# Kernel tuning notes

Hardware: AMD Instinct MI355X
Metric: run time of the kernel (lower is better)

## Reference

```python
import jax, jax.numpy as jnp
import numpy as np

WORDS_CNT = 34835
EMBED_DIM = 512
NEG = -1e30  # stand-in for -inf that is safe under autodiff


def setup_inputs() -> dict:
    key = jax.random.key(0)
    k1, k2, k3, k4, k5 = jax.random.split(key, 5)
    B, Tt, Td = 2048, 30, 150
    title = jax.random.randint(k1, (B, Tt), 0, WORDS_CNT + 1, dtype=jnp.int64)
    desc = jax.random.randint(k2, (B, Td), 0, WORDS_CNT + 1, dtype=jnp.int64)
    t_len = jax.random.randint(k3, (B,), 0, Tt + 1, dtype=jnp.int64)
    d_len = jax.random.randint(k4, (B,), 0, Td + 1, dtype=jnp.int64)
    word2vec = jax.random.normal(k5, (WORDS_CNT + 1, EMBED_DIM), dtype=jnp.float32)
    word2vec = word2vec.at[0].set(0.0)  # padding_idx=0
    return {"title": title, "desc": desc, "t_len": t_len, "d_len": d_len,
            "mode": 0, "word2vec": word2vec}


def _pool(vec, lens):
    # vec: [B, T, D], lens: [B] -> (max_pool [B, D], mean_pool [B, D])
    T = vec.shape[1]
    mask = (jnp.arange(T)[None, :] < lens[:, None])  # [B, T]
    m3 = mask[:, :, None]
    mx = jnp.max(jnp.where(m3, vec, NEG), axis=1)
    nonempty = (lens > 0)[:, None]
    mx = jnp.where(nonempty, mx, 0.0)
    denom = jnp.maximum(lens, 1).astype(vec.dtype)[:, None]
    mean = jnp.sum(jnp.where(m3, vec, 0.0), axis=1) / denom
    mean = jnp.where(nonempty, mean, 0.0)
    return mx, mean


def reference(title, desc, t_len, d_len, mode, word2vec):
    title_vec = word2vec[title]  # [B, Tt, D]
    desc_vec = word2vec[desc]    # [B, Td, D]
    t_max, t_avg = _pool(title_vec, t_len)
    d_max, d_avg = _pool(desc_vec, d_len)
    return jnp.concatenate([t_max, d_max, t_avg, d_avg], axis=1)  # [B, 4*D]
```

## Files before the change

kernel.cpp:

```cpp
#include <hip/hip_runtime.h>

#define TT 30
#define TD 150
#define NEGV -1e30f

__global__ __launch_bounds__(128) void swem_pool_kernel(
    const int* __restrict__ title, const int* __restrict__ desc,
    const int* __restrict__ t_len, const int* __restrict__ d_len,
    const float4* __restrict__ w2v, float4* __restrict__ out)
{
    __shared__ int s_idx[TT + TD];
    const int b = blockIdx.x;
    const int tid = threadIdx.x;

    if (tid < TT) s_idx[tid] = title[b * TT + tid];
    for (int i = tid; i < TD; i += 128) s_idx[TT + i] = desc[b * TD + i];
    __syncthreads();

    const int tl = t_len[b];
    const int dl = d_len[b];

    float4 mx = make_float4(NEGV, NEGV, NEGV, NEGV);
    float4 sm = make_float4(0.f, 0.f, 0.f, 0.f);
    for (int t = 0; t < tl; ++t) {
        const float4 v = w2v[(size_t)s_idx[t] * 128 + tid];
        mx.x = fmaxf(mx.x, v.x); mx.y = fmaxf(mx.y, v.y);
        mx.z = fmaxf(mx.z, v.z); mx.w = fmaxf(mx.w, v.w);
        sm.x += v.x; sm.y += v.y; sm.z += v.z; sm.w += v.w;
    }
    float4 tmax, tavg;
    if (tl > 0) {
        const float inv = 1.0f / (float)tl;
        tmax = mx;
        tavg = make_float4(sm.x * inv, sm.y * inv, sm.z * inv, sm.w * inv);
    } else {
        tmax = make_float4(0.f, 0.f, 0.f, 0.f);
        tavg = make_float4(0.f, 0.f, 0.f, 0.f);
    }

    mx = make_float4(NEGV, NEGV, NEGV, NEGV);
    sm = make_float4(0.f, 0.f, 0.f, 0.f);
    for (int t = 0; t < dl; ++t) {
        const float4 v = w2v[(size_t)s_idx[TT + t] * 128 + tid];
        mx.x = fmaxf(mx.x, v.x); mx.y = fmaxf(mx.y, v.y);
        mx.z = fmaxf(mx.z, v.z); mx.w = fmaxf(mx.w, v.w);
        sm.x += v.x; sm.y += v.y; sm.z += v.z; sm.w += v.w;
    }
    float4 dmax, davg;
    if (dl > 0) {
        const float inv = 1.0f / (float)dl;
        dmax = mx;
        davg = make_float4(sm.x * inv, sm.y * inv, sm.z * inv, sm.w * inv);
    } else {
        dmax = make_float4(0.f, 0.f, 0.f, 0.f);
        davg = make_float4(0.f, 0.f, 0.f, 0.f);
    }

    float4* orow = out + (size_t)b * 512;
    orow[tid]       = tmax;
    orow[128 + tid] = dmax;
    orow[256 + tid] = tavg;
    orow[384 + tid] = davg;
}

extern "C" void kernel_launch(void* const* d_in, const int* in_sizes, int n_in,
                              void* d_out, int out_size, void* d_ws, size_t ws_size,
                              hipStream_t stream) {
    const int* title = (const int*)d_in[0];
    const int* desc  = (const int*)d_in[1];
    const int* t_len = (const int*)d_in[2];
    const int* d_len = (const int*)d_in[3];
    const float4* w2v = (const float4*)d_in[5];

    float4* out = (float4*)d_out;

    const int B = in_sizes[2];
    swem_pool_kernel<<<B, 128, 0, stream>>>(title, desc, t_len, d_len, w2v, out);
}
```

Measured before the change: 148.9 us.

## Split title/desc into separate blocks and parallelize token loop across four groups

Launches a 2D grid so title and description pooling run in separate blocks. Each block uses 512 threads split into four groups that stride over tokens, then combines their partial max and sum through shared memory. The aim is more memory-level parallelism and fewer serial dependent gathers per thread, which should hide latency better. The cost is an extra shared-memory reduction and barrier, plus some idle groups on short title sequences.

```diff
diff --git a/kernel.cpp b/kernel.cpp
--- a/kernel.cpp
+++ b/kernel.cpp
@@ -3,64 +3,70 @@
 #define TT 30
 #define TD 150
 #define NEGV -1e30f
+#define NGRP 4
+#define LANES 128
 
-__global__ __launch_bounds__(128) void swem_pool_kernel(
+__global__ __launch_bounds__(512) void swem_pool_kernel(
     const int* __restrict__ title, const int* __restrict__ desc,
     const int* __restrict__ t_len, const int* __restrict__ d_len,
     const float4* __restrict__ w2v, float4* __restrict__ out)
 {
-    __shared__ int s_idx[TT + TD];
-    const int b = blockIdx.x;
-    const int tid = threadIdx.x;
+    __shared__ int s_idx[TD];
+    __shared__ float red[8][NGRP][LANES];
 
-    if (tid < TT) s_idx[tid] = title[b * TT + tid];
-    for (int i = tid; i < TD; i += 128) s_idx[TT + i] = desc[b * TD + i];
+    const int b    = blockIdx.x;
+    const int seg  = blockIdx.y;
+    const int tid  = threadIdx.x;
+    const int lane = tid & (LANES - 1);
+    const int grp  = tid >> 7;
+
+    const int* toks   = seg ? (desc + b * TD) : (title + b * TT);
+    const int  maxlen = seg ? TD : TT;
+    const int  len    = seg ? d_len[b] : t_len[b];
+
+    for (int i = tid; i < maxlen; i += 512) s_idx[i] = toks[i];
     __syncthreads();
-
-    const int tl = t_len[b];
-    const int dl = d_len[b];
 
     float4 mx = make_float4(NEGV, NEGV, NEGV, NEGV);
     float4 sm = make_float4(0.f, 0.f, 0.f, 0.f);
-    for (int t = 0; t < tl; ++t) {
-        const float4 v = w2v[(size_t)s_idx[t] * 128 + tid];
+    #pragma unroll 4
+    for (int t = grp; t < len; t += NGRP) {
+        const float4 v = w2v[(size_t)s_idx[t] * 128 + lane];
         mx.x = fmaxf(mx.x, v.x); mx.y = fmaxf(mx.y, v.y);
         mx.z = fmaxf(mx.z, v.z); mx.w = fmaxf(mx.w, v.w);
         sm.x += v.x; sm.y += v.y; sm.z += v.z; sm.w += v.w;
     }
-    float4 tmax, tavg;
-    if (tl > 0) {
-        const float inv = 1.0f / (float)tl;
-        tmax = mx;
-        tavg = make_float4(sm.x * inv, sm.y * inv, sm.z * inv, sm.w * inv);
-    } else {
-        tmax = make_float4(0.f, 0.f, 0.f, 0.f);
-        tavg = make_float4(0.f, 0.f, 0.f, 0.f);
-    }
 
-    mx = make_float4(NEGV, NEGV, NEGV, NEGV);
-    sm = make_float4(0.f, 0.f, 0.f, 0.f);
-    for (int t = 0; t < dl; ++t) {
-        const float4 v = w2v[(size_t)s_idx[TT + t] * 128 + tid];
-        mx.x = fmaxf(mx.x, v.x); mx.y = fmaxf(mx.y, v.y);
-        mx.z = fmaxf(mx.z, v.z); mx.w = fmaxf(mx.w, v.w);
-        sm.x += v.x; sm.y += v.y; sm.z += v.z; sm.w += v.w;
-    }
-    float4 dmax, davg;
-    if (dl > 0) {
-        const float inv = 1.0f / (float)dl;
-        dmax = mx;
-        davg = make_float4(sm.x * inv, sm.y * inv, sm.z * inv, sm.w * inv);
-    } else {
-        dmax = make_float4(0.f, 0.f, 0.f, 0.f);
-        davg = make_float4(0.f, 0.f, 0.f, 0.f);
-    }
+    red[0][grp][lane] = mx.x; red[1][grp][lane] = mx.y;
+    red[2][grp][lane] = mx.z; red[3][grp][lane] = mx.w;
+    red[4][grp][lane] = sm.x; red[5][grp][lane] = sm.y;
+    red[6][grp][lane] = sm.z; red[7][grp][lane] = sm.w;
+    __syncthreads();
 
     float4* orow = out + (size_t)b * 512;
-    orow[tid]       = tmax;
-    orow[128 + tid] = dmax;
-    orow[256 + tid] = tavg;
-    orow[384 + tid] = davg;
+
+    if (grp == 0) {
+        float4 r;
+        r.x = fmaxf(fmaxf(red[0][0][lane], red[0][1][lane]),
+                    fmaxf(red[0][2][lane], red[0][3][lane]));
+        r.y = fmaxf(fmaxf(red[1][0][lane], red[1][1][lane]),
+                    fmaxf(red[1][2][lane], red[1][3][lane]));
+        r.z = fmaxf(fmaxf(red[2][0][lane], red[2][1][lane]),
+                    fmaxf(red[2][2][lane], red[2][3][lane]));
+        r.w = fmaxf(fmaxf(red[3][0][lane], red[3][1][lane]),
+                    fmaxf(red[3][2][lane], red[3][3][lane]));
+        if (len == 0) r = make_float4(0.f, 0.f, 0.f, 0.f);
+        orow[seg * 128 + lane] = r;
+    } else if (grp == 1) {
+        const float inv = 1.0f / (float)(len > 0 ? len : 1);
+        float4 r;
+        r.x = (red[4][0][lane] + red[4][1][lane] + red[4][2][lane] + red[4][3][lane]) * inv;
+        r.y = (red[5][0][lane] + red[5][1][lane] + red[5][2][lane] + red[5][3][lane]) * inv;
+        r.z = (red[6][0][lane] + red[6][1][lane] + red[6][2][lane] + red[6][3][lane]) * inv;
+        r.w = (red[7][0][lane] + red[7][1][lane] + red[7][2][lane] + red[7][3][lane]) * inv;
+        if (len == 0) r = make_float4(0.f, 0.f, 0.f, 0.f);
+        orow[256 + seg * 128 + lane] = r;
+    }
 }
 
 extern "C" void kernel_launch(void* const* d_in, const int* in_sizes, int n_in,
@@ -73,7 +79,8 @@
     const float4* w2v = (const float4*)d_in[5];
 
     float4* out = (float4*)d_out;
+    const int B = in_sizes[2];
 
-    const int B = in_sizes[2];
-    swem_pool_kernel<<<B, 128, 0, stream>>>(title, desc, t_len, d_len, w2v, out);
+    dim3 grid(B, 2);
+    swem_pool_kernel<<<grid, 512, 0, stream>>>(title, desc, t_len, d_len, w2v, out);
 }
```

Result: no change. 148.6 us (-0.2%).

## Split title and desc pooling into separate blocks and unroll gather loop by 8

Applied to the files above, without the earlier changes.

Launches a 2D grid so that one block pools the title tokens and another pools the description tokens for each batch row, doubling the number of blocks. It also unrolls the token gather loop by eight so each thread has several independent row loads in flight. Both changes aim to hide gather latency, which is the main cost in this memory-bound embedding lookup. The trade-off is more blocks, load imbalance between the short title blocks and the long description blocks, and extra register pressure from the unrolled loads.

```diff
diff --git a/kernel.cpp b/kernel.cpp
--- a/kernel.cpp
+++ b/kernel.cpp
@@ -9,58 +9,58 @@
     const int* __restrict__ t_len, const int* __restrict__ d_len,
     const float4* __restrict__ w2v, float4* __restrict__ out)
 {
-    __shared__ int s_idx[TT + TD];
-    const int b = blockIdx.x;
+    __shared__ int s_idx[TD];
+
+    const int b   = blockIdx.x;
+    const int seg = blockIdx.y;
     const int tid = threadIdx.x;
 
-    if (tid < TT) s_idx[tid] = title[b * TT + tid];
-    for (int i = tid; i < TD; i += 128) s_idx[TT + i] = desc[b * TD + i];
+    const int* toks   = seg ? (desc + b * TD) : (title + b * TT);
+    const int  maxlen = seg ? TD : TT;
+    const int  len    = seg ? d_len[b] : t_len[b];
+
+    for (int i = tid; i < maxlen; i += 128) s_idx[i] = toks[i];
     __syncthreads();
-
-    const int tl = t_len[b];
-    const int dl = d_len[b];
 
     float4 mx = make_float4(NEGV, NEGV, NEGV, NEGV);
     float4 sm = make_float4(0.f, 0.f, 0.f, 0.f);
-    for (int t = 0; t < tl; ++t) {
+
+#define ACC(v) \
+    mx.x = fmaxf(mx.x, v.x); mx.y = fmaxf(mx.y, v.y); \
+    mx.z = fmaxf(mx.z, v.z); mx.w = fmaxf(mx.w, v.w); \
+    sm.x += v.x; sm.y += v.y; sm.z += v.z; sm.w += v.w;
+
+    int t = 0;
+    for (; t + 8 <= len; t += 8) {
+        const float4 v0 = w2v[(size_t)s_idx[t + 0] * 128 + tid];
+        const float4 v1 = w2v[(size_t)s_idx[t + 1] * 128 + tid];
+        const float4 v2 = w2v[(size_t)s_idx[t + 2] * 128 + tid];
+        const float4 v3 = w2v[(size_t)s_idx[t + 3] * 128 + tid];
+        const float4 v4 = w2v[(size_t)s_idx[t + 4] * 128 + tid];
+        const float4 v5 = w2v[(size_t)s_idx[t + 5] * 128 + tid];
+        const float4 v6 = w2v[(size_t)s_idx[t + 6] * 128 + tid];
+        const float4 v7 = w2v[(size_t)s_idx[t + 7] * 128 + tid];
+        ACC(v0) ACC(v1) ACC(v2) ACC(v3) ACC(v4) ACC(v5) ACC(v6) ACC(v7)
+    }
+    for (; t < len; ++t) {
         const float4 v = w2v[(size_t)s_idx[t] * 128 + tid];
-        mx.x = fmaxf(mx.x, v.x); mx.y = fmaxf(mx.y, v.y);
-        mx.z = fmaxf(mx.z, v.z); mx.w = fmaxf(mx.w, v.w);
-        sm.x += v.x; sm.y += v.y; sm.z += v.z; sm.w += v.w;
+        ACC(v)
     }
-    float4 tmax, tavg;
-    if (tl > 0) {
-        const float inv = 1.0f / (float)tl;
-        tmax = mx;
-        tavg = make_float4(sm.x * inv, sm.y * inv, sm.z * inv, sm.w * inv);
+#undef ACC
+
+    float4 rmax, ravg;
+    if (len > 0) {
+        const float inv = 1.0f / (float)len;
+        rmax = mx;
+        ravg = make_float4(sm.x * inv, sm.y * inv, sm.z * inv, sm.w * inv);
     } else {
-        tmax = make_float4(0.f, 0.f, 0.f, 0.f);
-        tavg = make_float4(0.f, 0.f, 0.f, 0.f);
-    }
-
-    mx = make_float4(NEGV, NEGV, NEGV, NEGV);
-    sm = make_float4(0.f, 0.f, 0.f, 0.f);
-    for (int t = 0; t < dl; ++t) {
-        const float4 v = w2v[(size_t)s_idx[TT + t] * 128 + tid];
-        mx.x = fmaxf(mx.x, v.x); mx.y = fmaxf(mx.y, v.y);
-        mx.z = fmaxf(mx.z, v.z); mx.w = fmaxf(mx.w, v.w);
-        sm.x += v.x; sm.y += v.y; sm.z += v.z; sm.w += v.w;
-    }
-    float4 dmax, davg;
-    if (dl > 0) {
-        const float inv = 1.0f / (float)dl;
-        dmax = mx;
-        davg = make_float4(sm.x * inv, sm.y * inv, sm.z * inv, sm.w * inv);
-    } else {
-        dmax = make_float4(0.f, 0.f, 0.f, 0.f);
-        davg = make_float4(0.f, 0.f, 0.f, 0.f);
+        rmax = make_float4(0.f, 0.f, 0.f, 0.f);
+        ravg = make_float4(0.f, 0.f, 0.f, 0.f);
     }
 
     float4* orow = out + (size_t)b * 512;
-    orow[tid]       = tmax;
-    orow[128 + tid] = dmax;
-    orow[256 + tid] = tavg;
-    orow[384 + tid] = davg;
+    orow[seg * 128 + tid]       = rmax;
+    orow[256 + seg * 128 + tid] = ravg;
 }
 
 extern "C" void kernel_launch(void* const* d_in, const int* in_sizes, int n_in,
@@ -73,7 +73,8 @@
     const float4* w2v = (const float4*)d_in[5];
 
     float4* out = (float4*)d_out;
+    const int B = in_sizes[2];
 
-    const int B = in_sizes[2];
-    swem_pool_kernel<<<B, 128, 0, stream>>>(title, desc, t_len, d_len, w2v, out);
+    dim3 grid(B, 2);
+    swem_pool_kernel<<<grid, 128, 0, stream>>>(title, desc, t_len, d_len, w2v, out);
 }
```

After: 151.5 us. No clear change (+1.7%).
